# Kernel tuning notes

Measured on AMD Instinct MI355X. Metric: run time of the kernel, lower is better.

## Reference

```python
import jax, jax.numpy as jnp
import numpy as np

NUM_EXPERTS = 64
NOISE_STD = 1.0
CAPACITY = 32  # top-C items per expert (experts-choice routing)
D_MODEL = 512
NUM_GROUPS = 8
GROUP_SIZE = 2048


def _top_items_per_expert_dispatcher(gates):
    """Experts-choice dispatcher for one group.

    gates: (S, E) softmax gate values.
    Returns:
      dispatch: (E, C, S) one-hot selection of the top-C items per expert.
      combine:  (S, E, C) gate value if item s is expert e's c-th pick, else 0.
    """
    s = gates.shape[0]
    # Each expert picks its top-C items by gate value.
    _, top_idx = jax.lax.top_k(gates.T, CAPACITY)          # (E, C)
    dispatch = jax.nn.one_hot(top_idx, s, dtype=gates.dtype)  # (E, C, S)
    combine = jnp.einsum('se,ecs->sec', gates, dispatch)      # (S, E, C)
    return dispatch, combine


def setup_inputs() -> dict:
    key = jax.random.key(0)
    k1, k2 = jax.random.split(key)
    inputs = jax.random.normal(k1, (NUM_GROUPS, GROUP_SIZE, D_MODEL), dtype=jnp.float32)
    # Dense(num_experts, use_bias=False) kernel, lecun-normal-ish scale.
    W = jax.random.normal(k2, (D_MODEL, NUM_EXPERTS), dtype=jnp.float32) * (D_MODEL ** -0.5)
    return {"inputs": inputs, "W": W}


def reference(inputs, W):
    # Gating projection: (G, S, D) x (D, E) -> (G, S, E)
    logits = jnp.einsum('gsd,de->gse', inputs, W)
    # Noisy gating: noise_std scaled by 1/num_experts (as in the module).
    noise_scale = NOISE_STD / NUM_EXPERTS
    noise = noise_scale * jax.random.normal(jax.random.key(42), logits.shape, dtype=logits.dtype)
    gates = jax.nn.softmax(logits + noise, axis=-1)  # (G, S, E)
    # vmap the per-group top-items-per-expert dispatcher over groups.
    dispatch, combine = jax.vmap(_top_items_per_expert_dispatcher)(gates)
    return combine, dispatch
```

## Files before the change

kernel.cpp:

```cpp
#include <hip/hip_runtime.h>
#include <math.h>
#include <stdint.h>

#define NG 8
#define GS 2048
#define DM 512
#define NE 64
#define CAP 32
#define NROWS (NG * GS)
#define COMBINE_ELEMS (33554432ull)

#define N4 16777216
#define GATE_BLOCKS 512
#define XST 516
#define TBS 21

typedef float f32x4 __attribute__((ext_vector_type(4)));
typedef double f64x2 __attribute__((ext_vector_type(2)));
typedef double f64x4 __attribute__((ext_vector_type(4)));
typedef unsigned long long u64;

__device__ __forceinline__ void threefry2x32(uint32_t k0, uint32_t k1,
                                             uint32_t x0, uint32_t x1,
                                             uint32_t& o0, uint32_t& o1) {
  uint32_t ks[3] = {k0, k1, k0 ^ k1 ^ 0x1BD11BDAu};
  x0 += ks[0];
  x1 += ks[1];
  const uint32_t rot[2][4] = {{13u, 15u, 26u, 6u}, {17u, 29u, 16u, 24u}};
#pragma unroll
  for (int i = 0; i < 5; ++i) {
#pragma unroll
    for (int j = 0; j < 4; ++j) {
      uint32_t r = rot[i & 1][j];
      x0 += x1;
      x1 = (x1 << r) | (x1 >> (32u - r));
      x1 ^= x0;
    }
    x0 += ks[(i + 1) % 3];
    x1 += ks[(i + 2) % 3] + (uint32_t)(i + 1);
  }
  o0 = x0;
  o1 = x1;
}

__device__ __forceinline__ float erfinv_xla(float x) {
  float w = -log1pf(-x * x);
  float p;
  if (w < 5.0f) {
    w = w - 2.5f;
    p = 2.81022636e-08f;
    p = __fmaf_rn(p, w, 3.43273939e-07f);
    p = __fmaf_rn(p, w, -3.5233877e-06f);
    p = __fmaf_rn(p, w, -4.39150654e-06f);
    p = __fmaf_rn(p, w, 0.00021858087f);
    p = __fmaf_rn(p, w, -0.00125372503f);
    p = __fmaf_rn(p, w, -0.00417768164f);
    p = __fmaf_rn(p, w, 0.246640727f);
    p = __fmaf_rn(p, w, 1.50140941f);
  } else {
    w = sqrtf(w) - 3.0f;
    p = -0.000200214257f;
    p = __fmaf_rn(p, w, 0.000100950558f);
    p = __fmaf_rn(p, w, 0.00134934322f);
    p = __fmaf_rn(p, w, -0.00367342844f);
    p = __fmaf_rn(p, w, 0.00573950773f);
    p = __fmaf_rn(p, w, -0.0076224613f);
    p = __fmaf_rn(p, w, 0.00943887047f);
    p = __fmaf_rn(p, w, 1.00167406f);
    p = __fmaf_rn(p, w, 2.83297682f);
  }
  return p * x;
}

__device__ __forceinline__ float jax_normal(uint32_t idx) {
  uint32_t o0, o1;
  threefry2x32(0u, 42u, 0u, idx, o0, o1);
  uint32_t bits = o0 ^ o1;
  float f = __uint_as_float((bits >> 9) | 0x3f800000u) - 1.0f;
  const float lo = __uint_as_float(0xBF7FFFFFu);
  float v = fmaxf(lo, f * 2.0f + lo);
  return __uint_as_float(0x3FB504F3u) * erfinv_xla(v);
}

__global__ __launch_bounds__(256) void wprep_kernel(
    const float* __restrict__ Wt, double* __restrict__ Wd) {
  const int i = blockIdx.x * 256 + threadIdx.x;
  const int t = i & 3, i15 = (i >> 2) & 15, row = i >> 6;
  Wd[i] = (double)Wt[row * NE + t * 16 + i15];
}

__global__ __launch_bounds__(256) void zero_kernel(f32x4* __restrict__ p) {
  const int b = blockIdx.x * 1024 + threadIdx.x;
  const f32x4 z = {0.f, 0.f, 0.f, 0.f};
#pragma unroll
  for (int j = 0; j < 4; ++j) p[b + j * 256] = z;
}

__global__ __launch_bounds__(128) void gate_kernel(
    const float* __restrict__ x,
    const double* __restrict__ Wd,
    float* __restrict__ gatesT) {
  __shared__ float xs[32 * XST];
  const int gid = blockIdx.x;
  const int tid = threadIdx.x;
  const int l = tid & 63;
  const int w = tid >> 6;
  const int row0b = gid * 32;
  const int row0 = row0b + w * 16;

  const int i15 = l & 15;
  const int k4 = l >> 4;

  f64x4 dr = {0., 0., 0., 0.};
  dr = __builtin_amdgcn_mfma_f64_16x16x4f64((double)i15, 0.25, dr, 0, 0, 0);
  int perm[4];
#pragma unroll
  for (int r = 0; r < 4; ++r) perm[r] = ((int)(dr[r] + 0.5)) & 15;

#pragma unroll 8
  for (int i = tid; i < 4096; i += 128) {
    const int r = i >> 7, c = (i & 127) << 2;
    *(f32x4*)&xs[r * XST + c] =
        *(const f32x4*)&x[(size_t)(row0b + r) * DM + c];
  }
  __syncthreads();

  f64x4 acc[4] = {{0., 0., 0., 0.}, {0., 0., 0., 0.},
                  {0., 0., 0., 0.}, {0., 0., 0., 0.}};
  const float* xrow = &xs[(w * 16 + i15) * XST + k4];
  const double* wl = Wd + k4 * 64 + i15 * 4;
  f64x2 b01 = *(const f64x2*)(wl + 0);
  f64x2 b23 = *(const f64x2*)(wl + 2);
#pragma unroll 4
  for (int kk = 0; kk < 128; ++kk) {
    const int nk = (kk + 1) & 127;
    const f64x2 nb01 = *(const f64x2*)(wl + nk * 256 + 0);
    const f64x2 nb23 = *(const f64x2*)(wl + nk * 256 + 2);
    const double a = (double)xrow[kk * 4];
    acc[0] = __builtin_amdgcn_mfma_f64_16x16x4f64(a, b01[0], acc[0], 0, 0, 0);
    acc[1] = __builtin_amdgcn_mfma_f64_16x16x4f64(a, b01[1], acc[1], 0, 0, 0);
    acc[2] = __builtin_amdgcn_mfma_f64_16x16x4f64(a, b23[0], acc[2], 0, 0, 0);
    acc[3] = __builtin_amdgcn_mfma_f64_16x16x4f64(a, b23[1], acc[3], 0, 0, 0);
    b01 = nb01;
    b23 = nb23;
  }

  float gatef[4][4];
#pragma unroll
  for (int r = 0; r < 4; ++r) {
    const int row = row0 + perm[r];
    double v[4];
    double m = -1.0e300;
#pragma unroll
    for (int t = 0; t < 4; ++t) {
      const float logit = (float)acc[t][r];
      const float noised =
          logit + 0.015625f * jax_normal((uint32_t)(row * NE + 16 * t + i15));
      v[t] = (double)noised;
      m = fmax(m, v[t]);
    }
#pragma unroll
    for (int off = 1; off < 16; off <<= 1) m = fmax(m, __shfl_xor(m, off, 64));
    double s = 0.0;
#pragma unroll
    for (int t = 0; t < 4; ++t) {
      v[t] = exp(v[t] - m);
      s += v[t];
    }
#pragma unroll
    for (int off = 1; off < 16; off <<= 1) s += __shfl_xor(s, off, 64);
#pragma unroll
    for (int t = 0; t < 4; ++t) gatef[t][r] = (float)(v[t] / s);
  }

  float* tb = xs + w * (NE * TBS);
#pragma unroll
  for (int t = 0; t < 4; ++t)
#pragma unroll
    for (int r = 0; r < 4; ++r)
      tb[(16 * t + i15) * TBS + perm[r]] = gatef[t][r];

  const int g = row0 >> 11;
  const int s0 = row0 & (GS - 1);
  float* drow = gatesT + ((size_t)(g * NE + l)) * GS + s0;
#pragma unroll
  for (int c = 0; c < 4; ++c) {
    f32x4 o;
#pragma unroll
    for (int i = 0; i < 4; ++i) o[i] = tb[l * TBS + 4 * c + i];
    *(f32x4*)&drow[4 * c] = o;
  }
}

__global__ __launch_bounds__(64) void topk_kernel(
    const float* __restrict__ gatesT,
    float* __restrict__ out) {
  const int ge = blockIdx.x;
  const int g = ge >> 6;
  const int e = ge & 63;
  const int lane = threadIdx.x;

  const float* base = gatesT + (size_t)ge * GS;
  u64 K[32];
#pragma unroll
  for (int k = 0; k < 8; ++k) {
    const f32x4 t = *(const f32x4*)(base + k * 256 + lane * 4);
#pragma unroll
    for (int i = 0; i < 4; ++i) {
      const int s = k * 256 + lane * 4 + i;
      K[k * 4 + i] = ((u64)__float_as_uint(t[i]) << 32) | (u64)(2047 - s);
    }
  }

#pragma unroll
  for (int k = 2; k <= 32; k <<= 1) {
#pragma unroll
    for (int d = k >> 1; d > 0; d >>= 1) {
#pragma unroll
      for (int j = 0; j < 32; ++j) {
        const int ixj = j ^ d;
        if (ixj > j) {
          const bool asc = ((j & k) == 0);
          const u64 a = K[j], b = K[ixj];
          const bool sw = asc ? (a > b) : (a < b);
          K[j] = sw ? b : a;
          K[ixj] = sw ? a : b;
        }
      }
    }
  }

#pragma unroll
  for (int m = 1; m < 64; m <<= 1) {
    u64 tmp[32];
#pragma unroll
    for (int j = 0; j < 32; ++j) tmp[j] = __shfl_xor(K[31 - j], m, 64);
#pragma unroll
    for (int j = 0; j < 32; ++j) K[j] = (K[j] > tmp[j]) ? K[j] : tmp[j];
#pragma unroll
    for (int d = 16; d > 0; d >>= 1) {
#pragma unroll
      for (int j = 0; j < 32; ++j) {
        if ((j & d) == 0) {
          const u64 a = K[j], b = K[j | d];
          const bool sw = (a > b);
          K[j] = sw ? b : a;
          K[j | d] = sw ? a : b;
        }
      }
    }
  }

  float* combine = out;
  float* dispatch = out + COMBINE_ELEMS;
#pragma unroll
  for (int c = 0; c < CAP; ++c) {
    if (lane == c) {
      const u64 key = K[31 - c];
      const float v = __uint_as_float((uint32_t)(key >> 32));
      const int s = 2047 - (int)(key & 0x7FFull);
      combine[(((size_t)(g * GS + s)) * NE + e) * CAP + c] = v;
      dispatch[(((size_t)(g * NE + e)) * CAP + c) * GS + s] = 1.0f;
    }
  }
}

extern "C" void kernel_launch(void* const* d_in, const int* in_sizes, int n_in,
                              void* d_out, int out_size, void* d_ws,
                              size_t ws_size, hipStream_t stream) {
  (void)in_sizes; (void)n_in; (void)ws_size; (void)out_size;
  const float* x = (const float*)d_in[0];
  const float* Wt = (const float*)d_in[1];
  float* out = (float*)d_out;
  float* gatesT = (float*)d_ws;
  double* Wd = (double*)((char*)d_ws + ((size_t)NROWS * NE * 4));

  wprep_kernel<<<128, 256, 0, stream>>>(Wt, Wd);
  zero_kernel<<<N4 / 1024, 256, 0, stream>>>((f32x4*)out);
  gate_kernel<<<GATE_BLOCKS, 128, 0, stream>>>(x, Wd, gatesT);
  topk_kernel<<<NG * NE, 64, 0, stream>>>(gatesT, out);
}
```

Baseline: 120.3 us.

## Replace zero-fill plus scatter with dense writer kernel for combine and dispatch

Drops the separate zero-fill of the 128 MB output. The top-k kernel now stores only its selected keys to workspace, and a new writer kernel emits every combine and dispatch element once, zeros included, as vectorized stores. This removes the zero pass and the scattered single-element writes. The cost is an extra kernel launch and a workspace round trip for the selections, and the combine stores are strided per expert.

```diff
diff --git a/kernel.cpp b/kernel.cpp
--- a/kernel.cpp
+++ b/kernel.cpp
@@ -10,7 +10,6 @@
 #define NROWS (NG * GS)
 #define COMBINE_ELEMS (33554432ull)
 
-#define N4 16777216
 #define GATE_BLOCKS 512
 #define XST 516
 #define TBS 21
@@ -89,13 +88,6 @@
   Wd[i] = (double)Wt[row * NE + t * 16 + i15];
 }
 
-__global__ __launch_bounds__(256) void zero_kernel(f32x4* __restrict__ p) {
-  const int b = blockIdx.x * 1024 + threadIdx.x;
-  const f32x4 z = {0.f, 0.f, 0.f, 0.f};
-#pragma unroll
-  for (int j = 0; j < 4; ++j) p[b + j * 256] = z;
-}
-
 __global__ __launch_bounds__(128) void gate_kernel(
     const float* __restrict__ x,
     const double* __restrict__ Wd,
@@ -192,12 +184,10 @@
   }
 }
 
-__global__ __launch_bounds__(64) void topk_kernel(
+__global__ __launch_bounds__(64) void topsel_kernel(
     const float* __restrict__ gatesT,
-    float* __restrict__ out) {
+    u64* __restrict__ topsel) {
   const int ge = blockIdx.x;
-  const int g = ge >> 6;
-  const int e = ge & 63;
   const int lane = threadIdx.x;
 
   const float* base = gatesT + (size_t)ge * GS;
@@ -251,17 +241,65 @@
     }
   }
 
-  float* combine = out;
-  float* dispatch = out + COMBINE_ELEMS;
 #pragma unroll
   for (int c = 0; c < CAP; ++c) {
-    if (lane == c) {
-      const u64 key = K[31 - c];
-      const float v = __uint_as_float((uint32_t)(key >> 32));
-      const int s = 2047 - (int)(key & 0x7FFull);
-      combine[(((size_t)(g * GS + s)) * NE + e) * CAP + c] = v;
-      dispatch[(((size_t)(g * NE + e)) * CAP + c) * GS + s] = 1.0f;
-    }
+    if (lane == c) topsel[(size_t)ge * CAP + c] = K[31 - c];
+  }
+}
+
+__global__ __launch_bounds__(256) void writer_kernel(
+    const u64* __restrict__ topsel,
+    float* __restrict__ out) {
+  __shared__ int sel_s[CAP];
+  __shared__ float sel_v[CAP];
+  __shared__ unsigned char c_of_s[GS];
+  const int b = blockIdx.x;
+  const int ge = b >> 2, q = b & 3;
+  const int g = ge >> 6, e = ge & 63;
+  const int tid = threadIdx.x;
+  const int lane = tid & 63, w = tid >> 6;
+
+  ((u64*)c_of_s)[tid] = ~0ull;
+  if (tid < CAP) {
+    const u64 key = topsel[(size_t)ge * CAP + tid];
+    sel_s[tid] = 2047 - (int)(key & 0x7FFull);
+    sel_v[tid] = __uint_as_float((uint32_t)(key >> 32));
+  }
+  __syncthreads();
+  if (tid < CAP) c_of_s[sel_s[tid]] = (unsigned char)tid;
+  __syncthreads();
+
+  float* drow_base = out + COMBINE_ELEMS + (size_t)ge * CAP * GS;
+#pragma unroll
+  for (int rr = 0; rr < 2; ++rr) {
+    const int c = 8 * q + 2 * w + rr;
+    const int sc = sel_s[c];
+    float* rowp = drow_base + (size_t)c * GS;
+#pragma unroll
+    for (int j = 0; j < 8; ++j) {
+      const int pos = j * 256 + lane * 4;
+      f32x4 v;
+      v[0] = (sc == pos + 0) ? 1.0f : 0.0f;
+      v[1] = (sc == pos + 1) ? 1.0f : 0.0f;
+      v[2] = (sc == pos + 2) ? 1.0f : 0.0f;
+      v[3] = (sc == pos + 3) ? 1.0f : 0.0f;
+      *(f32x4*)&rowp[pos] = v;
+    }
+  }
+
+  const int pos = (lane & 7) * 4;
+#pragma unroll
+  for (int it = 0; it < 16; ++it) {
+    const int s = 512 * q + 128 * w + 8 * it + (lane >> 3);
+    const int c = c_of_s[s];
+    const float val = (c != 255) ? sel_v[c & 31] : 0.0f;
+    const int d = c - pos;
+    f32x4 v;
+    v[0] = (d == 0) ? val : 0.0f;
+    v[1] = (d == 1) ? val : 0.0f;
+    v[2] = (d == 2) ? val : 0.0f;
+    v[3] = (d == 3) ? val : 0.0f;
+    *(f32x4*)&out[(((size_t)(g * GS + s)) * NE + e) * CAP + pos] = v;
   }
 }
 
@@ -274,9 +312,10 @@
   float* out = (float*)d_out;
   float* gatesT = (float*)d_ws;
   double* Wd = (double*)((char*)d_ws + ((size_t)NROWS * NE * 4));
+  u64* topsel = (u64*)((char*)Wd + (size_t)DM * NE * 8);
 
   wprep_kernel<<<128, 256, 0, stream>>>(Wt, Wd);
-  zero_kernel<<<N4 / 1024, 256, 0, stream>>>((f32x4*)out);
   gate_kernel<<<GATE_BLOCKS, 128, 0, stream>>>(x, Wd, gatesT);
-  topk_kernel<<<NG * NE, 64, 0, stream>>>(gatesT, out);
-}
+  topsel_kernel<<<NG * NE, 64, 0, stream>>>(gatesT, topsel);
+  writer_kernel<<<NG * NE * 4, 256, 0, stream>>>(topsel, out);
+}
```

After: 119.4 us. Within noise of the previous version (-0.7%).
